# Kernel tuning notes

Hardware: AMD Instinct MI355X
Metric: run time of the kernel (lower is better)

## Reference

```python
import jax, jax.numpy as jnp
import numpy as np
import math

B, T, D_MODEL, N_HEAD = 2, 2048, 1024, 16
NUM_BUCKETS, MAX_DIST = 32, 128
D_HEAD = D_MODEL // N_HEAD


def _relative_position_bucket(rel_pos, num_buckets=NUM_BUCKETS, max_distance=MAX_DIST):
    # bidirectional=True branch of the torch code
    nb = num_buckets // 2
    buckets = (rel_pos > 0).astype(jnp.int32) * nb
    rel_pos = jnp.abs(rel_pos)
    max_exact = nb // 2
    is_small = rel_pos < max_exact
    # guard log(0); masked out by is_small anyway
    large = max_exact + (
        jnp.log(jnp.maximum(rel_pos, 1).astype(jnp.float32) / max_exact)
        / math.log(max_distance / max_exact) * (nb - max_exact)
    ).astype(jnp.int32)
    large = jnp.minimum(large, nb - 1)
    return buckets + jnp.where(is_small, rel_pos, large)


def compute_bias(rel_bias, q_len, kv_len):
    qp = jnp.arange(q_len, dtype=jnp.int32)[:, None]
    kp = jnp.arange(kv_len, dtype=jnp.int32)[None, :]
    buckets = _relative_position_bucket(kp - qp)          # [Tq, Tkv]
    vals = rel_bias[buckets]                              # [Tq, Tkv, H]
    return jnp.transpose(vals, (2, 0, 1))                 # [H, Tq, Tkv]


def setup_inputs() -> dict:
    key = jax.random.key(0)
    ks = jax.random.split(key, 9)
    inp = {
        'q': jax.random.normal(ks[0], (B, T, D_MODEL), jnp.float32),
        'k': jax.random.normal(ks[1], (B, T, D_MODEL), jnp.float32),
        'v': jax.random.normal(ks[2], (B, T, D_MODEL), jnp.float32),
        'mask': jax.random.randint(ks[3], (B, T, T), 0, 2, jnp.int32),
        'Wq': jax.random.normal(ks[4], (D_MODEL, D_MODEL), jnp.float32) * 0.02,
        'Wk': jax.random.normal(ks[5], (D_MODEL, D_MODEL), jnp.float32) * 0.02,
        'Wv': jax.random.normal(ks[6], (D_MODEL, D_MODEL), jnp.float32) * 0.02,
        'Wfc': jax.random.normal(ks[7], (D_MODEL, D_MODEL), jnp.float32) * 0.02,
        'rel_bias': jax.random.normal(ks[8], (NUM_BUCKETS, N_HEAD), jnp.float32) * 0.02,
    }
    return inp


def reference(q, k, v, mask, Wq, Wk, Wv, Wfc, rel_bias):
    b, tq, _ = q.shape
    tkv = k.shape[1]
    qh = (q @ Wq).reshape(b, tq, N_HEAD, D_HEAD)
    kh = (k @ Wk).reshape(b, tkv, N_HEAD, D_HEAD)
    vh = (v @ Wv).reshape(b, tkv, N_HEAD, D_HEAD)
    attn = jnp.einsum('blhd,bthd->bhlt', qh, kh) / np.sqrt(D_HEAD).astype(np.float32)
    position_bias = compute_bias(rel_bias, tq, tkv)       # [H, Tq, Tkv]
    attn = attn + position_bias[None]                     # broadcast over batch
    attn = jnp.where(mask[:, None] == 0, -1e9, attn)
    attn = jax.nn.softmax(attn, axis=-1)                  # dropout: eval mode (identity)
    out = jnp.einsum('bhlt,bthd->blhd', attn, vh).reshape(b, tq, D_MODEL)
    out = out @ Wfc
    return out, position_bias[:, None]                    # bias returned as [H,1,Tq,Tkv] like torch
```

## Files before the change

### kernel.cpp

```cpp
#include <hip/hip_runtime.h>
#include <math.h>

#define TT 2048
#define BB 2
#define HH 16
#define DMODEL 1024
#define NREL 4095

typedef __attribute__((ext_vector_type(8)))  _Float16 half8;
typedef __attribute__((ext_vector_type(4)))  _Float16 half4;
typedef __attribute__((ext_vector_type(16))) float    f32x16;
typedef __attribute__((ext_vector_type(4)))  int      int4v;

__device__ __forceinline__ f32x16 zero16() {
    f32x16 v;
#pragma unroll
    for (int i = 0; i < 16; ++i) v[i] = 0.f;
    return v;
}

__device__ __forceinline__ unsigned pkh(float a, float b) {
    union { _Float16 h[2]; unsigned u; } x;
    x.h[0] = (_Float16)a; x.h[1] = (_Float16)b;
    return x.u;
}

__device__ __forceinline__ void gload16(const void* g, void* l) {
    __builtin_amdgcn_global_load_lds(
        (const __attribute__((address_space(1))) void*)g,
        (__attribute__((address_space(3))) void*)l, 16, 0, 0);
}

__device__ __forceinline__ int rel_bucket(int rel) {
    int base = rel > 0 ? 16 : 0;
    int r = rel < 0 ? -rel : rel;
    int lb;
    if (r < 8)       lb = r;
    else if (r < 12) lb = 8;
    else if (r < 16) lb = 9;
    else if (r < 23) lb = 10;
    else if (r < 32) lb = 11;
    else if (r < 46) lb = 12;
    else if (r < 64) lb = 13;
    else if (r < 91) lb = 14;
    else             lb = 15;
    return base + lb;
}

__global__ __launch_bounds__(256) void prep_kernel(
    const float* __restrict__ q, const float* __restrict__ k,
    const float* __restrict__ v, const int* __restrict__ mask,
    const float* __restrict__ W0, const float* __restrict__ W1,
    const float* __restrict__ W2, const float* __restrict__ W3,
    const float* __restrict__ rel_bias,
    _Float16* __restrict__ q16, _Float16* __restrict__ k16,
    _Float16* __restrict__ v16, _Float16* __restrict__ WT,
    float* __restrict__ btable, unsigned* __restrict__ mb)
{
    __shared__ float t[64][65];
    int bid = blockIdx.x, tid = threadIdx.x;
    if (bid < 256) {
        int idx = bid * 256 + tid;
        if (idx < HH * NREL) {
            int h = idx / NREL, ri = idx % NREL;
            btable[idx] = rel_bias[rel_bucket(ri - (TT - 1)) * HH + h];
        }
    } else if (bid < 1280) {
        int zz = (bid - 256) >> 8, inner = (bid - 256) & 255;
        const float* src = zz == 0 ? W0 : zz == 1 ? W1 : zz == 2 ? W2 : W3;
        _Float16* dst = WT + (size_t)zz * DMODEL * DMODEL;
        int k0 = (inner >> 4) * 64, n0 = (inner & 15) * 64;
        int r = tid >> 4, c4 = (tid & 15) * 4;
#pragma unroll
        for (int i = 0; i < 4; ++i) {
            float4 vv = *(const float4*)(src + (size_t)(k0 + r + 16 * i) * DMODEL + n0 + c4);
            t[r + 16 * i][c4] = vv.x; t[r + 16 * i][c4 + 1] = vv.y;
            t[r + 16 * i][c4 + 2] = vv.z; t[r + 16 * i][c4 + 3] = vv.w;
        }
        __syncthreads();
        int rn = tid >> 2, ck = (tid & 3) * 16;
        half8 h0, h1;
#pragma unroll
        for (int j = 0; j < 8; ++j) h0[j] = (_Float16)t[ck + j][rn];
#pragma unroll
        for (int j = 0; j < 8; ++j) h1[j] = (_Float16)t[ck + 8 + j][rn];
        *(half8*)(dst + (size_t)(n0 + rn) * DMODEL + k0 + ck) = h0;
        *(half8*)(dst + (size_t)(n0 + rn) * DMODEL + k0 + ck + 8) = h1;
    } else if (bid < 7424) {
        int zz = (bid - 1280) >> 11, inner = (bid - 1280) & 2047;
        const float* src = zz == 0 ? q : zz == 1 ? k : v;
        _Float16* dst = zz == 0 ? q16 : zz == 1 ? k16 : v16;
        int i = inner * 256 + tid;
        const float4* in4 = (const float4*)src;
        float4 v0 = in4[(size_t)i * 2], v1 = in4[(size_t)i * 2 + 1];
        half8 h = {(_Float16)v0.x, (_Float16)v0.y, (_Float16)v0.z, (_Float16)v0.w,
                   (_Float16)v1.x, (_Float16)v1.y, (_Float16)v1.z, (_Float16)v1.w};
        *(half8*)(dst + (size_t)i * 8) = h;
    } else {
        int g = (bid - 7424) * 256 + tid;
        int vv = mask[g];
        unsigned long long bal = __ballot(vv != 0);
        if ((g & 63) == 0) {
            int word = g >> 5;
            mb[word]     = (unsigned)bal;
            mb[word + 1] = (unsigned)(bal >> 32);
        }
    }
}

__global__ __launch_bounds__(256, 4) void gemm_proj3(
    const _Float16* __restrict__ q16, const _Float16* __restrict__ k16,
    const _Float16* __restrict__ v16, const _Float16* __restrict__ WT,
    _Float16* __restrict__ qhf, _Float16* __restrict__ khf,
    _Float16* __restrict__ vtf, int zbase)
{
    __shared__ __align__(16) char lds[32768];
    int z = zbase + blockIdx.z;
    const _Float16* A  = z == 0 ? q16 : z == 1 ? k16 : v16;
    const _Float16* Bt = WT + (size_t)z * DMODEL * DMODEL;
    int bm = blockIdx.x * 128, bn = blockIdx.y * 128;
    int tid = threadIdx.x;
    int wv = tid >> 6, lane = tid & 63, lo = lane & 31, hi = lane >> 5;
    int wr = wv >> 1, wc = wv & 1;
    int srow = wv * 32 + (lane >> 3);
    int scol = (lane & 7) * 8;

    f32x16 acc[2][2];
    acc[0][0] = zero16(); acc[0][1] = zero16();
    acc[1][0] = zero16(); acc[1][1] = zero16();

    for (int kt = 0; kt < 16; ++kt) {
#pragma unroll
        for (int t = 0; t < 4; ++t) {
            gload16(A  + (size_t)(bm + srow + t * 8) * DMODEL + kt * 64 + scol,
                    lds + wv * 4096 + t * 1024);
            gload16(Bt + (size_t)(bn + srow + t * 8) * DMODEL + kt * 64 + scol,
                    lds + 16384 + wv * 4096 + t * 1024);
        }
        __syncthreads();
#pragma unroll
        for (int kk = 0; kk < 4; ++kk) {
            int cs = 2 * kk + hi;
            half8 a[2], b[2];
#pragma unroll
            for (int i = 0; i < 2; ++i) {
                a[i] = *(const half8*)(lds + (wr * 64 + i * 32 + lo) * 128 + cs * 16);
                b[i] = *(const half8*)(lds + 16384 + (wc * 64 + i * 32 + lo) * 128 + cs * 16);
            }
            acc[0][0] = __builtin_amdgcn_mfma_f32_32x32x16_f16(a[0], b[0], acc[0][0], 0, 0, 0);
            acc[0][1] = __builtin_amdgcn_mfma_f32_32x32x16_f16(a[0], b[1], acc[0][1], 0, 0, 0);
            acc[1][0] = __builtin_amdgcn_mfma_f32_32x32x16_f16(a[1], b[0], acc[1][0], 0, 0, 0);
            acc[1][1] = __builtin_amdgcn_mfma_f32_32x32x16_f16(a[1], b[1], acc[1][1], 0, 0, 0);
        }
        __syncthreads();
    }

    if (z < 2) {
        _Float16* C = z == 0 ? qhf : khf;
#pragma unroll
        for (int j = 0; j < 2; ++j) {
            int n = bn + wc * 64 + j * 32 + lo;
            int h = n >> 6, d = n & 63;
#pragma unroll
            for (int i = 0; i < 2; ++i) {
                int mb2 = bm + wr * 64 + i * 32 + 4 * hi;
#pragma unroll
                for (int r = 0; r < 16; ++r) {
                    int m = mb2 + (r & 3) + 8 * (r >> 2);
                    int b = m >> 11, t = m & (TT - 1);
                    C[((size_t)(b * HH + h) * TT + t) * 64 + d] = (_Float16)acc[i][j][r];
                }
            }
        }
    } else {
#pragma unroll
        for (int j = 0; j < 2; ++j) {
            int n = bn + wc * 64 + j * 32 + lo;
            int h = n >> 6, d = n & 63;
#pragma unroll
            for (int i = 0; i < 2; ++i) {
                int mb2 = bm + wr * 64 + i * 32 + 4 * hi;
                int b = mb2 >> 11, tb = mb2 & (TT - 1);
#pragma unroll
                for (int r4 = 0; r4 < 4; ++r4) {
                    half4 hv = {(_Float16)acc[i][j][4 * r4 + 0], (_Float16)acc[i][j][4 * r4 + 1],
                                (_Float16)acc[i][j][4 * r4 + 2], (_Float16)acc[i][j][4 * r4 + 3]};
                    *(half4*)(vtf + ((size_t)(b * HH + h) * 64 + d) * TT + tb + 8 * r4) = hv;
                }
            }
        }
    }
}

__global__ __launch_bounds__(256) void attn_mfma(
    const _Float16* __restrict__ qh, const _Float16* __restrict__ kh,
    const _Float16* __restrict__ vt, const unsigned* __restrict__ maskbits,
    const float* __restrict__ btable, _Float16* __restrict__ Oout)
{
    int bid = blockIdx.x;
    int xcd = bid & 7, j = bid >> 3;
    int qt = j & 15, bh = xcd + 8 * (j >> 4);
    int h = bh & 15, b = bh >> 4;
    int tid = threadIdx.x;
    int wv = tid >> 6, lane = tid & 63, lo = lane & 31, hi = lane >> 5;
    int q0 = qt * 128 + wv * 32;

    const size_t bhoff = (size_t)(b * HH + h);
    const _Float16* Q = qh + (bhoff * TT + q0) * 64;
    const _Float16* K = kh + bhoff * TT * 64;
    const _Float16* V = vt + bhoff * 64 * TT;

    half8 qf[4];
#pragma unroll
    for (int c = 0; c < 4; ++c)
        qf[c] = *(const half8*)(Q + (size_t)lo * 64 + c * 16 + hi * 8);

    const float* bt = btable + h * NREL + (TT - 1) - (q0 + lo) + 4 * hi;
    const unsigned* mw = maskbits + ((size_t)b * TT + q0 + lo) * 64;

    f32x16 acco0 = zero16(), acco1 = zero16();
    float m = -INFINITY, l = 0.f;

    for (int kt = 0; kt < TT / 64; ++kt) {
        int k0 = kt * 64;
        half8 kf[2][4];
#pragma unroll
        for (int g = 0; g < 2; ++g)
#pragma unroll
            for (int c = 0; c < 4; ++c)
                kf[g][c] = *(const half8*)(K + (size_t)(k0 + 32 * g + lo) * 64 + c * 16 + hi * 8);
        unsigned wm0 = mw[2 * kt], wm1 = mw[2 * kt + 1];

        f32x16 accs0 = zero16(), accs1 = zero16();
        __builtin_amdgcn_s_setprio(1);
#pragma unroll
        for (int c = 0; c < 4; ++c) {
            accs0 = __builtin_amdgcn_mfma_f32_32x32x16_f16(kf[0][c], qf[c], accs0, 0, 0, 0);
            accs1 = __builtin_amdgcn_mfma_f32_32x32x16_f16(kf[1][c], qf[c], accs1, 0, 0, 0);
        }
        __builtin_amdgcn_s_setprio(0);

        float p[2][16];
        unsigned ws0 = wm0 >> (hi * 4), ws1 = wm1 >> (hi * 4);
#pragma unroll
        for (int r = 0; r < 16; ++r) {
            int sh = (r & 3) + 8 * (r >> 2);
            float s0 = fmaf(accs0[r], 0.125f, bt[k0 + sh]);
            float s1 = fmaf(accs1[r], 0.125f, bt[k0 + sh + 32]);
            p[0][r] = ((ws0 >> sh) & 1) ? s0 : -1e9f;
            p[1][r] = ((ws1 >> sh) & 1) ? s1 : -1e9f;
        }

        float tm = p[0][0];
#pragma unroll
        for (int g = 0; g < 2; ++g)
#pragma unroll
            for (int r = 0; r < 16; ++r) tm = fmaxf(tm, p[g][r]);
        tm = fmaxf(tm, __shfl_xor(tm, 32));
        float mnew = fmaxf(m, tm);
        float corr = __expf(m - mnew);
        float rs = 0.f;
#pragma unroll
        for (int g = 0; g < 2; ++g)
#pragma unroll
            for (int r = 0; r < 16; ++r) {
                p[g][r] = __expf(p[g][r] - mnew);
                rs += p[g][r];
            }
        rs += __shfl_xor(rs, 32);
        l = l * corr + rs; m = mnew;
#pragma unroll
        for (int r = 0; r < 16; ++r) { acco0[r] *= corr; acco1[r] *= corr; }

        half8 vf[2][4];
#pragma unroll
        for (int dg = 0; dg < 2; ++dg)
#pragma unroll
            for (int c = 0; c < 4; ++c)
                vf[dg][c] = *(const half8*)(V + (size_t)(32 * dg + lo) * TT + k0 + c * 16 + hi * 8);

        half8 pb[4];
#pragma unroll
        for (int g = 0; g < 2; ++g)
#pragma unroll
            for (int hc = 0; hc < 2; ++hc) {
                int r0 = hc * 8;
                unsigned w0 = pkh(p[g][r0 + 0], p[g][r0 + 1]);
                unsigned w2 = pkh(p[g][r0 + 4], p[g][r0 + 5]);
                asm("v_permlane32_swap_b32 %0, %1" : "+v"(w0), "+v"(w2));
                unsigned w1 = pkh(p[g][r0 + 2], p[g][r0 + 3]);
                unsigned w3 = pkh(p[g][r0 + 6], p[g][r0 + 7]);
                asm("v_permlane32_swap_b32 %0, %1" : "+v"(w1), "+v"(w3));
                union { int4v i; half8 hf; } cv;
                cv.i = (int4v){(int)w0, (int)w1, (int)w2, (int)w3};
                pb[2 * g + hc] = cv.hf;
            }

        __builtin_amdgcn_s_setprio(1);
#pragma unroll
        for (int c = 0; c < 4; ++c) {
            acco0 = __builtin_amdgcn_mfma_f32_32x32x16_f16(vf[0][c], pb[c], acco0, 0, 0, 0);
            acco1 = __builtin_amdgcn_mfma_f32_32x32x16_f16(vf[1][c], pb[c], acco1, 0, 0, 0);
        }
        __builtin_amdgcn_s_setprio(0);
    }

    float inv = 1.f / l;
    _Float16* op = Oout + (bhoff * TT + q0 + lo) * 64;
#pragma unroll
    for (int r4 = 0; r4 < 4; ++r4) {
        int d0 = 8 * r4 + 4 * hi;
        half4 h0 = {(_Float16)(acco0[4 * r4 + 0] * inv), (_Float16)(acco0[4 * r4 + 1] * inv),
                    (_Float16)(acco0[4 * r4 + 2] * inv), (_Float16)(acco0[4 * r4 + 3] * inv)};
        *(half4*)(op + d0) = h0;
        half4 h1 = {(_Float16)(acco1[4 * r4 + 0] * inv), (_Float16)(acco1[4 * r4 + 1] * inv),
                    (_Float16)(acco1[4 * r4 + 2] * inv), (_Float16)(acco1[4 * r4 + 3] * inv)};
        *(half4*)(op + d0 + 32) = h1;
    }
}

__global__ __launch_bounds__(256) void fc_bias_kernel(
    const _Float16* __restrict__ O, const _Float16* __restrict__ Bt,
    float* __restrict__ out0, const float* __restrict__ btable,
    float* __restrict__ out1)
{
    __shared__ __align__(16) char lds[32768];
    int bid = blockIdx.x, tid = threadIdx.x;
    if (bid >= 256) {
        const int n4 = HH * TT * TT / 4, stride = 2048 * 256;
        for (int i4 = (bid - 256) * 256 + tid; i4 < n4; i4 += stride) {
            int i = i4 * 4;
            int kk = i & (TT - 1);
            int qq = (i >> 11) & (TT - 1);
            int hh2 = i >> 22;
            const float* btp = btable + hh2 * NREL + (kk - qq + (TT - 1));
            float4 vv = make_float4(btp[0], btp[1], btp[2], btp[3]);
            reinterpret_cast<float4*>(out1)[i4] = vv;
        }
        return;
    }
    int bm = (bid & 31) * 128, bn = (bid >> 5) * 128;
    int wv = tid >> 6, lane = tid & 63, lo = lane & 31, hi = lane >> 5;
    int wr = wv >> 1, wc = wv & 1;
    int srow = wv * 32 + (lane >> 3);
    int scol = (lane & 7) * 8;
    int bb = bm >> 11, tbase = bm & (TT - 1);

    f32x16 acc[2][2];
    acc[0][0] = zero16(); acc[0][1] = zero16();
    acc[1][0] = zero16(); acc[1][1] = zero16();

    for (int kt = 0; kt < 16; ++kt) {
        const _Float16* Ab = O + ((size_t)(bb * HH + kt) * TT + tbase) * 64;
#pragma unroll
        for (int t = 0; t < 4; ++t) {
            gload16(Ab + (size_t)(srow + t * 8) * 64 + scol,
                    lds + wv * 4096 + t * 1024);
            gload16(Bt + (size_t)(bn + srow + t * 8) * DMODEL + kt * 64 + scol,
                    lds + 16384 + wv * 4096 + t * 1024);
        }
        __syncthreads();
#pragma unroll
        for (int kk = 0; kk < 4; ++kk) {
            int cs = 2 * kk + hi;
            half8 a[2], b[2];
#pragma unroll
            for (int i = 0; i < 2; ++i) {
                a[i] = *(const half8*)(lds + (wr * 64 + i * 32 + lo) * 128 + cs * 16);
                b[i] = *(const half8*)(lds + 16384 + (wc * 64 + i * 32 + lo) * 128 + cs * 16);
            }
            acc[0][0] = __builtin_amdgcn_mfma_f32_32x32x16_f16(a[0], b[0], acc[0][0], 0, 0, 0);
            acc[0][1] = __builtin_amdgcn_mfma_f32_32x32x16_f16(a[0], b[1], acc[0][1], 0, 0, 0);
            acc[1][0] = __builtin_amdgcn_mfma_f32_32x32x16_f16(a[1], b[0], acc[1][0], 0, 0, 0);
            acc[1][1] = __builtin_amdgcn_mfma_f32_32x32x16_f16(a[1], b[1], acc[1][1], 0, 0, 0);
        }
        __syncthreads();
    }

#pragma unroll
    for (int j = 0; j < 2; ++j) {
        int n = bn + wc * 64 + j * 32 + lo;
#pragma unroll
        for (int i = 0; i < 2; ++i) {
            int mb2 = bm + wr * 64 + i * 32 + 4 * hi;
#pragma unroll
            for (int r = 0; r < 16; ++r) {
                int m = mb2 + (r & 3) + 8 * (r >> 2);
                out0[(size_t)m * DMODEL + n] = acc[i][j][r];
            }
        }
    }
}

extern "C" void kernel_launch(void* const* d_in, const int* in_sizes, int n_in,
                              void* d_out, int out_size, void* d_ws, size_t ws_size,
                              hipStream_t stream) {
    const float* q        = (const float*)d_in[0];
    const float* k        = (const float*)d_in[1];
    const float* v        = (const float*)d_in[2];
    const int*   mask     = (const int*)  d_in[3];
    const float* Wq       = (const float*)d_in[4];
    const float* Wk       = (const float*)d_in[5];
    const float* Wv       = (const float*)d_in[6];
    const float* Wfc      = (const float*)d_in[7];
    const float* rel_bias = (const float*)d_in[8];

    float* out0 = (float*)d_out;
    float* out1 = out0 + (size_t)BB * TT * DMODEL;

    char* w = (char*)d_ws;
    _Float16* q16 = (_Float16*)(w);
    _Float16* k16 = (_Float16*)(w + ((size_t)8  << 20));
    _Float16* v16 = (_Float16*)(w + ((size_t)16 << 20));
    _Float16* qhf = (_Float16*)(w + ((size_t)24 << 20));
    _Float16* khf = (_Float16*)(w + ((size_t)32 << 20));
    _Float16* WT  = (_Float16*)(w + ((size_t)40 << 20));
    float*    btable = (float*)(w + ((size_t)48 << 20));
    unsigned* mbits  = (unsigned*)(w + ((size_t)48 << 20) + ((size_t)1 << 19));
    bool big = ws_size >= ((size_t)58 << 20);
    _Float16* vtf = big ? (_Float16*)(w + ((size_t)49 << 20) + ((size_t)1 << 19))
                        : k16;
    _Float16* O = q16;

    prep_kernel<<<dim3(40192), dim3(256), 0, stream>>>(
        q, k, v, mask, Wq, Wk, Wv, Wfc, rel_bias, q16, k16, v16, WT, btable, mbits);

    if (big) {
        gemm_proj3<<<dim3(32, 8, 3), dim3(256), 0, stream>>>(q16, k16, v16, WT,
                                                             qhf, khf, vtf, 0);
    } else {
        gemm_proj3<<<dim3(32, 8, 1), dim3(256), 0, stream>>>(q16, k16, v16, WT, qhf, khf, vtf, 0);
        gemm_proj3<<<dim3(32, 8, 1), dim3(256), 0, stream>>>(q16, k16, v16, WT, qhf, khf, vtf, 1);
        gemm_proj3<<<dim3(32, 8, 1), dim3(256), 0, stream>>>(q16, k16, v16, WT, qhf, khf, vtf, 2);
    }

    attn_mfma<<<dim3(BB * HH * 16), dim3(256), 0, stream>>>(
        qhf, khf, vtf, mbits, btable, O);

    fc_bias_kernel<<<dim3(2304), dim3(256), 0, stream>>>(
        O, WT + (size_t)3 * DMODEL * DMODEL, out0, btable, out1);
}
```

Measured before the change: 291.2 us.

## Double-buffer LDS in projection/FC GEMMs and use constant bias for distant tiles

Both GEMM kernels now use a double-buffered 64KB LDS. The next K-tile is staged while the current one is computed, so global-load latency overlaps with MFMA work. In the attention kernel, tiles whose relative distance is far enough that the position bucket saturates take a single scalar bias value instead of gathering per-element bias from the table. The larger LDS footprint and the dropped occupancy hint may lower waves per CU in the GEMMs, and the final iteration issues one redundant tile load.

```diff
diff --git a/kernel.cpp b/kernel.cpp
--- a/kernel.cpp
+++ b/kernel.cpp
@@ -108,13 +108,13 @@
     }
 }
 
-__global__ __launch_bounds__(256, 4) void gemm_proj3(
+__global__ __launch_bounds__(256) void gemm_proj3(
     const _Float16* __restrict__ q16, const _Float16* __restrict__ k16,
     const _Float16* __restrict__ v16, const _Float16* __restrict__ WT,
     _Float16* __restrict__ qhf, _Float16* __restrict__ khf,
     _Float16* __restrict__ vtf, int zbase)
 {
-    __shared__ __align__(16) char lds[32768];
+    __shared__ __align__(16) char lds[65536];
     int z = zbase + blockIdx.z;
     const _Float16* A  = z == 0 ? q16 : z == 1 ? k16 : v16;
     const _Float16* Bt = WT + (size_t)z * DMODEL * DMODEL;
@@ -124,34 +124,45 @@
     int wr = wv >> 1, wc = wv & 1;
     int srow = wv * 32 + (lane >> 3);
     int scol = (lane & 7) * 8;
+    const _Float16* Abase = A  + (size_t)(bm + srow) * DMODEL + scol;
+    const _Float16* Bbase = Bt + (size_t)(bn + srow) * DMODEL + scol;
 
     f32x16 acc[2][2];
     acc[0][0] = zero16(); acc[0][1] = zero16();
     acc[1][0] = zero16(); acc[1][1] = zero16();
 
-    for (int kt = 0; kt < 16; ++kt) {
+    auto stage = [&](int buf, int kt) {
 #pragma unroll
         for (int t = 0; t < 4; ++t) {
-            gload16(A  + (size_t)(bm + srow + t * 8) * DMODEL + kt * 64 + scol,
-                    lds + wv * 4096 + t * 1024);
-            gload16(Bt + (size_t)(bn + srow + t * 8) * DMODEL + kt * 64 + scol,
-                    lds + 16384 + wv * 4096 + t * 1024);
-        }
-        __syncthreads();
+            gload16(Abase + (size_t)t * 8 * DMODEL + kt * 64, lds + buf + wv * 4096 + t * 1024);
+            gload16(Bbase + (size_t)t * 8 * DMODEL + kt * 64, lds + buf + 16384 + wv * 4096 + t * 1024);
+        }
+    };
+    auto compute = [&](int buf) {
 #pragma unroll
         for (int kk = 0; kk < 4; ++kk) {
             int cs = 2 * kk + hi;
             half8 a[2], b[2];
 #pragma unroll
             for (int i = 0; i < 2; ++i) {
-                a[i] = *(const half8*)(lds + (wr * 64 + i * 32 + lo) * 128 + cs * 16);
-                b[i] = *(const half8*)(lds + 16384 + (wc * 64 + i * 32 + lo) * 128 + cs * 16);
+                a[i] = *(const half8*)(lds + buf + (wr * 64 + i * 32 + lo) * 128 + cs * 16);
+                b[i] = *(const half8*)(lds + buf + 16384 + (wc * 64 + i * 32 + lo) * 128 + cs * 16);
             }
             acc[0][0] = __builtin_amdgcn_mfma_f32_32x32x16_f16(a[0], b[0], acc[0][0], 0, 0, 0);
             acc[0][1] = __builtin_amdgcn_mfma_f32_32x32x16_f16(a[0], b[1], acc[0][1], 0, 0, 0);
             acc[1][0] = __builtin_amdgcn_mfma_f32_32x32x16_f16(a[1], b[0], acc[1][0], 0, 0, 0);
             acc[1][1] = __builtin_amdgcn_mfma_f32_32x32x16_f16(a[1], b[1], acc[1][1], 0, 0, 0);
         }
+    };
+
+    stage(0, 0);
+    __syncthreads();
+    for (int kt = 0; kt < 16; kt += 2) {
+        stage(32768, kt + 1);
+        compute(0);
+        __syncthreads();
+        stage(0, kt + 2 < 16 ? kt + 2 : 15);
+        compute(32768);
         __syncthreads();
     }
 
@@ -216,6 +227,8 @@
         qf[c] = *(const half8*)(Q + (size_t)lo * 64 + c * 16 + hi * 8);
 
     const float* bt = btable + h * NREL + (TT - 1) - (q0 + lo) + 4 * hi;
+    const float bias_l = btable[h * NREL];
+    const float bias_r = btable[h * NREL + NREL - 1];
     const unsigned* mw = maskbits + ((size_t)b * TT + q0 + lo) * 64;
 
     f32x16 acco0 = zero16(), acco1 = zero16();
@@ -240,33 +253,47 @@
         }
         __builtin_amdgcn_s_setprio(0);
 
-        float p[2][16];
         unsigned ws0 = wm0 >> (hi * 4), ws1 = wm1 >> (hi * 4);
-#pragma unroll
-        for (int r = 0; r < 16; ++r) {
-            int sh = (r & 3) + 8 * (r >> 2);
-            float s0 = fmaf(accs0[r], 0.125f, bt[k0 + sh]);
-            float s1 = fmaf(accs1[r], 0.125f, bt[k0 + sh + 32]);
-            p[0][r] = ((ws0 >> sh) & 1) ? s0 : -1e9f;
-            p[1][r] = ((ws1 >> sh) & 1) ? s1 : -1e9f;
-        }
-
-        float tm = p[0][0];
-#pragma unroll
-        for (int g = 0; g < 2; ++g)
-#pragma unroll
-            for (int r = 0; r < 16; ++r) tm = fmaxf(tm, p[g][r]);
+        bool rconst = k0 > q0 + 121;
+        bool lconst = k0 + 63 < q0 - 90;
+        if (rconst | lconst) {
+            float bc = rconst ? bias_r : bias_l;
+#pragma unroll
+            for (int r = 0; r < 16; ++r) {
+                int sh = (r & 3) + 8 * (r >> 2);
+                float s0 = fmaf(accs0[r], 0.125f, bc);
+                float s1 = fmaf(accs1[r], 0.125f, bc);
+                accs0[r] = ((ws0 >> sh) & 1) ? s0 : -1e9f;
+                accs1[r] = ((ws1 >> sh) & 1) ? s1 : -1e9f;
+            }
+        } else {
+#pragma unroll
+            for (int r = 0; r < 16; ++r) {
+                int sh = (r & 3) + 8 * (r >> 2);
+                float s0 = fmaf(accs0[r], 0.125f, bt[k0 + sh]);
+                float s1 = fmaf(accs1[r], 0.125f, bt[k0 + sh + 32]);
+                accs0[r] = ((ws0 >> sh) & 1) ? s0 : -1e9f;
+                accs1[r] = ((ws1 >> sh) & 1) ? s1 : -1e9f;
+            }
+        }
+
+        float tm = accs0[0];
+#pragma unroll
+        for (int r = 1; r < 16; ++r) tm = fmaxf(tm, accs0[r]);
+#pragma unroll
+        for (int r = 0; r < 16; ++r) tm = fmaxf(tm, accs1[r]);
         tm = fmaxf(tm, __shfl_xor(tm, 32));
         float mnew = fmaxf(m, tm);
         float corr = __expf(m - mnew);
         float rs = 0.f;
 #pragma unroll
-        for (int g = 0; g < 2; ++g)
-#pragma unroll
-            for (int r = 0; r < 16; ++r) {
-                p[g][r] = __expf(p[g][r] - mnew);
-                rs += p[g][r];
-            }
+        for (int r = 0; r < 16; ++r) {
+            accs0[r] = __expf(accs0[r] - mnew); rs += accs0[r];
+        }
+#pragma unroll
+        for (int r = 0; r < 16; ++r) {
+            accs1[r] = __expf(accs1[r] - mnew); rs += accs1[r];
+        }
         rs += __shfl_xor(rs, 32);
         l = l * corr + rs; m = mnew;
 #pragma unroll
@@ -285,11 +312,19 @@
 #pragma unroll
             for (int hc = 0; hc < 2; ++hc) {
                 int r0 = hc * 8;
-                unsigned w0 = pkh(p[g][r0 + 0], p[g][r0 + 1]);
-                unsigned w2 = pkh(p[g][r0 + 4], p[g][r0 + 5]);
+                float p0 = g ? accs1[r0 + 0] : accs0[r0 + 0];
+                float p1 = g ? accs1[r0 + 1] : accs0[r0 + 1];
+                float p2 = g ? accs1[r0 + 2] : accs0[r0 + 2];
+                float p3 = g ? accs1[r0 + 3] : accs0[r0 + 3];
+                float p4 = g ? accs1[r0 + 4] : accs0[r0 + 4];
+                float p5 = g ? accs1[r0 + 5] : accs0[r0 + 5];
+                float p6 = g ? accs1[r0 + 6] : accs0[r0 + 6];
+                float p7 = g ? accs1[r0 + 7] : accs0[r0 + 7];
+                unsigned w0 = pkh(p0, p1);
+                unsigned w2 = pkh(p4, p5);
                 asm("v_permlane32_swap_b32 %0, %1" : "+v"(w0), "+v"(w2));
-                unsigned w1 = pkh(p[g][r0 + 2], p[g][r0 + 3]);
-                unsigned w3 = pkh(p[g][r0 + 6], p[g][r0 + 7]);
+                unsigned w1 = pkh(p2, p3);
+                unsigned w3 = pkh(p6, p7);
                 asm("v_permlane32_swap_b32 %0, %1" : "+v"(w1), "+v"(w3));
                 union { int4v i; half8 hf; } cv;
                 cv.i = (int4v){(int)w0, (int)w1, (int)w2, (int)w3};
@@ -324,7 +359,7 @@
     float* __restrict__ out0, const float* __restrict__ btable,
     float* __restrict__ out1)
 {
-    __shared__ __align__(16) char lds[32768];
+    __shared__ __align__(16) char lds[65536];
     int bid = blockIdx.x, tid = threadIdx.x;
     if (bid >= 256) {
         const int n4 = HH * TT * TT / 4, stride = 2048 * 256;
@@ -345,35 +380,45 @@
     int srow = wv * 32 + (lane >> 3);
     int scol = (lane & 7) * 8;
     int bb = bm >> 11, tbase = bm & (TT - 1);
+    const _Float16* Abase = O + ((size_t)(bb * HH) * TT + tbase + srow) * 64 + scol;
+    const _Float16* Bbase = Bt + (size_t)(bn + srow) * DMODEL + scol;
 
     f32x16 acc[2][2];
     acc[0][0] = zero16(); acc[0][1] = zero16();
     acc[1][0] = zero16(); acc[1][1] = zero16();
 
-    for (int kt = 0; kt < 16; ++kt) {
-        const _Float16* Ab = O + ((size_t)(bb * HH + kt) * TT + tbase) * 64;
+    auto stage = [&](int buf, int kt) {
 #pragma unroll
         for (int t = 0; t < 4; ++t) {
-            gload16(Ab + (size_t)(srow + t * 8) * 64 + scol,
-                    lds + wv * 4096 + t * 1024);
-            gload16(Bt + (size_t)(bn + srow + t * 8) * DMODEL + kt * 64 + scol,
-                    lds + 16384 + wv * 4096 + t * 1024);
-        }
-        __syncthreads();
+            gload16(Abase + (size_t)kt * TT * 64 + (size_t)t * 8 * 64, lds + buf + wv * 4096 + t * 1024);
+            gload16(Bbase + (size_t)t * 8 * DMODEL + kt * 64, lds + buf + 16384 + wv * 4096 + t * 1024);
+        }
+    };
+    auto compute = [&](int buf) {
 #pragma unroll
         for (int kk = 0; kk < 4; ++kk) {
             int cs = 2 * kk + hi;
             half8 a[2], b[2];
 #pragma unroll
             for (int i = 0; i < 2; ++i) {
-                a[i] = *(const half8*)(lds + (wr * 64 + i * 32 + lo) * 128 + cs * 16);
-                b[i] = *(const half8*)(lds + 16384 + (wc * 64 + i * 32 + lo) * 128 + cs * 16);
+                a[i] = *(const half8*)(lds + buf + (wr * 64 + i * 32 + lo) * 128 + cs * 16);
+                b[i] = *(const half8*)(lds + buf + 16384 + (wc * 64 + i * 32 + lo) * 128 + cs * 16);
             }
             acc[0][0] = __builtin_amdgcn_mfma_f32_32x32x16_f16(a[0], b[0], acc[0][0], 0, 0, 0);
             acc[0][1] = __builtin_amdgcn_mfma_f32_32x32x16_f16(a[0], b[1], acc[0][1], 0, 0, 0);
             acc[1][0] = __builtin_amdgcn_mfma_f32_32x32x16_f16(a[1], b[0], acc[1][0], 0, 0, 0);
             acc[1][1] = __builtin_amdgcn_mfma_f32_32x32x16_f16(a[1], b[1], acc[1][1], 0, 0, 0);
         }
+    };
+
+    stage(0, 0);
+    __syncthreads();
+    for (int kt = 0; kt < 16; kt += 2) {
+        stage(32768, kt + 1);
+        compute(0);
+        __syncthreads();
+        stage(0, kt + 2 < 16 ? kt + 2 : 15);
+        compute(32768);
         __syncthreads();
     }
 
```

Result: faster. 284.9 us (-2.2%).
